# Performance work log

Hardware: AMD Instinct MI355X
Metric: run time of the kernel (lower is better)

Reference implementation:

```python
import jax, jax.numpy as jnp
import numpy as np

NUM_LABELS = 8  # static label-set size (mask values in [0, NUM_LABELS))


def setup_inputs() -> dict:
    key = jax.random.key(0)
    k1, k2, k3, k4 = jax.random.split(key, 4)
    B, C, H, W = 2, 256, 256, 256
    return {
        "c_feat": jax.random.normal(k1, (B, C, H, W), dtype=jnp.float32),
        "s_feat": jax.random.normal(k2, (B, C, H, W), dtype=jnp.float32),
        "c_mask": jax.random.randint(k3, (H, W), 0, NUM_LABELS, dtype=jnp.int64),
        "s_mask": jax.random.randint(k4, (H, W), 0, NUM_LABELS, dtype=jnp.int64),
    }


def reference(c_feat, s_feat, c_mask, s_mask):
    B, C, H, W = c_feat.shape
    cf = c_feat.reshape(B, C, H * W)            # [B, C, Nc]
    sf = s_feat.reshape(B, C, -1)               # [B, C, Ns]
    cm = c_mask.reshape(-1)                     # [Nc]
    sm = s_mask.reshape(-1)                     # [Ns]
    out = cf
    for label in range(NUM_LABELS):
        cw = (cm == label).astype(cf.dtype)     # 0/1 weights over content pixels
        sw = (sm == label).astype(sf.dtype)
        a = cw.sum()
        b = sw.sum()
        # guide-label heuristic from compute_label_info
        guide = (a > 10) & (b > 10) & (a < 10 * b) & (b < 10 * a)
        # masked content mean / centered features (zeros outside the label group)
        c_mean = (cf * cw).sum(-1) / a          # [B, C]
        c_res = (cf - c_mean[:, :, None]) * cw  # [B, C, Nc]
        cov_c = jnp.einsum('bcn,bdn->bce'.replace('e', 'd'), c_res, c_res) / (a - 1.0)
        Lc = jnp.linalg.inv(jnp.linalg.cholesky(cov_c))   # whitening (inverse Cholesky)
        # masked style statistics
        s_mean = (sf * sw).sum(-1) / b          # [B, C]
        s_res = (sf - s_mean[:, :, None]) * sw  # [B, C, Ns]
        cov_s = jnp.einsum('bcn,bdn->bcd', s_res, s_res) / (b - 1.0)
        Ls = jnp.linalg.cholesky(cov_s)                   # coloring Cholesky
        T = jnp.einsum('bcd,bde->bce', Ls, Lc)            # [B, C, C]
        colored = jnp.einsum('bce,ben->bcn', T, cf - c_mean[:, :, None]) + s_mean[:, :, None]
        sel = guide & (cm == label)             # scatter only guided label pixels
        out = jnp.where(sel[None, None, :], colored, out)
    return out.reshape(B, C, H, W)
```

## Files before the change

kernel.cpp:

```cpp
#include <hip/hip_runtime.h>
#include <stdint.h>

#define BB 2
#define CC 256
#define NN 65536
#define LL 8

#define M_CNTC 0
#define M_CNTS 8
#define M_OFFC 16
#define M_OFFS 24
#define M_CURC 32
#define M_CURS 40
#define M_GUIDE 48

typedef const __attribute__((address_space(1))) unsigned int* gp1_t;
typedef __attribute__((address_space(3))) unsigned int* lp3_t;

__device__ __forceinline__ void gload16(const float* g, float* l) {
    __builtin_amdgcn_global_load_lds((gp1_t)(const void*)g, (lp3_t)(void*)l, 16, 0, 0);
}

__global__ void k_hist(const int* __restrict__ cm, const int* __restrict__ sm,
                       int* __restrict__ meta)
{
    __shared__ int lc[LL], ls[LL];
    int t = threadIdx.x;
    if (t < LL) { lc[t] = 0; ls[t] = 0; }
    __syncthreads();
    int n = blockIdx.x * 256 + t;
    atomicAdd(&lc[cm[n] & 7], 1);
    atomicAdd(&ls[sm[n] & 7], 1);
    __syncthreads();
    if (t < LL) {
        atomicAdd(&meta[M_CNTC + t], lc[t]);
        atomicAdd(&meta[M_CNTS + t], ls[t]);
    }
}

__global__ void k_scan(int* __restrict__ meta)
{
    if (threadIdx.x == 0 && blockIdx.x == 0) {
        int oc = 0, os = 0;
        for (int l = 0; l < LL; l++) {
            meta[M_OFFC + l] = oc; meta[M_CURC + l] = oc;
            meta[M_OFFS + l] = os; meta[M_CURS + l] = os;
            oc += meta[M_CNTC + l];
            os += meta[M_CNTS + l];
        }
        for (int l = 0; l < LL; l++) {
            int a = meta[M_CNTC + l], b = meta[M_CNTS + l];
            meta[M_GUIDE + l] = (a > 10 && b > 10 && a < 10 * b && b < 10 * a) ? 1 : 0;
        }
    }
}

__global__ void k_dest(const int* __restrict__ cm, const int* __restrict__ sm,
                       int* __restrict__ meta, int* __restrict__ pdc, int* __restrict__ pds)
{
    int n = blockIdx.x * 256 + threadIdx.x;
    int lane = threadIdx.x & 63;
    unsigned long long below = (1ull << lane) - 1ull;
    int lc = cm[n] & 7, ls = sm[n] & 7;
    int dc = 0, dsv = 0;
    for (int lab = 0; lab < LL; lab++) {
        unsigned long long m = __ballot(lc == lab);
        if (m) {
            int leader = __ffsll((unsigned long long)m) - 1;
            int cntw = __popcll(m);
            int base = 0;
            if (lane == leader) base = atomicAdd(&meta[M_CURC + lab], cntw);
            base = __shfl(base, leader, 64);
            if (lc == lab) dc = base + __popcll(m & below);
        }
        unsigned long long m2 = __ballot(ls == lab);
        if (m2) {
            int leader = __ffsll((unsigned long long)m2) - 1;
            int cntw = __popcll(m2);
            int base = 0;
            if (lane == leader) base = atomicAdd(&meta[M_CURS + lab], cntw);
            base = __shfl(base, leader, 64);
            if (ls == lab) dsv = base + __popcll(m2 & below);
        }
    }
    pdc[n] = dc | (lc << 16);
    pds[n] = dsv | (ls << 16);
}

__global__ void k_gather(const float* __restrict__ feat, const int* __restrict__ pd,
                         float* __restrict__ X, float* __restrict__ sums)
{
    __shared__ float sacc[LL][256];
    int t = threadIdx.x;
    int c = blockIdx.y, b = blockIdx.z;
    int n0 = blockIdx.x * 8192;
    for (int r = 0; r < LL; r++) sacc[r][t] = 0.f;
    const float* row = feat + ((size_t)b * CC + c) * NN;
    float* Xrow = X + ((size_t)b * CC + c) * NN;
    for (int it = 0; it < 8; it++) {
        int n = n0 + it * 1024 + t * 4;
        float4 v = *(const float4*)(row + n);
        int4 pp = *(const int4*)(pd + n);
        int d0 = pp.x & 0xFFFF, l0 = pp.x >> 16;
        int d1 = pp.y & 0xFFFF, l1 = pp.y >> 16;
        int d2 = pp.z & 0xFFFF, l2 = pp.z >> 16;
        int d3 = pp.w & 0xFFFF, l3 = pp.w >> 16;
        Xrow[d0] = v.x; sacc[l0][t] += v.x;
        Xrow[d1] = v.y; sacc[l1][t] += v.y;
        Xrow[d2] = v.z; sacc[l2][t] += v.z;
        Xrow[d3] = v.w; sacc[l3][t] += v.w;
    }
    __syncthreads();
    int r = t >> 5, q = t & 31;
    float s = 0.f;
    for (int k = q; k < 256; k += 32) s += sacc[r][k];
    for (int off = 16; off; off >>= 1) s += __shfl_down(s, off, 32);
    if (q == 0) atomicAdd(&sums[((size_t)b * LL + r) * CC + c], s);
}

__global__ __launch_bounds__(256, 4) void k_syrk(const float* __restrict__ Xc, const float* __restrict__ Xs,
                                                 float* __restrict__ Raw, const int* __restrict__ meta)
{
    int z = blockIdx.z;
    int l = z & 7, b = (z >> 3) & 1, st = z >> 4;
    if (!meta[M_GUIDE + l]) return;
    int cnt = meta[(st ? M_CNTS : M_CNTC) + l];
    int off = meta[(st ? M_OFFS : M_OFFC) + l];
    int KCH = gridDim.x;
    int clen = (((cnt + KCH - 1) / KCH) + 31) & ~31;
    int p0 = off + blockIdx.x * clen;
    int lend = off + cnt;
    if (p0 >= lend) return;
    int pend = min(p0 + clen, lend);
    int y = blockIdx.y;
    int tR = (y >= 1) ? 128 : 0;
    int tC = (y == 2) ? 128 : 0;

    const float* Xb = (st ? Xs : Xc) + (size_t)b * CC * NN;

    __shared__ float As[32][132];
    __shared__ float Bs[32][132];

    int t = threadIdx.x;
    int ty = t >> 4, tx = t & 15;
    int sr = t & 31, sx = t >> 5;

    float acc[8][8];
#pragma unroll
    for (int i = 0; i < 8; i++)
#pragma unroll
        for (int j = 0; j < 8; j++) acc[i][j] = 0.f;

    for (int k0 = p0; k0 < pend; k0 += 32) {
        __syncthreads();
        int p = k0 + sx * 4;
#pragma unroll
        for (int pass = 0; pass < 4; pass++) {
            int row = pass * 32 + sr;
            const float* ap = Xb + (size_t)(tR + row) * NN + p;
            const float* bp = Xb + (size_t)(tC + row) * NN + p;
            float4 av = {0.f, 0.f, 0.f, 0.f}, bv = {0.f, 0.f, 0.f, 0.f};
            if (p + 3 < pend) { av = *(const float4*)ap; bv = *(const float4*)bp; }
            else if (p < pend) {
                int nleft = pend - p;
                for (int j = 0; j < nleft; j++) { ((float*)&av)[j] = ap[j]; ((float*)&bv)[j] = bp[j]; }
            }
            As[sx * 4 + 0][row] = av.x; As[sx * 4 + 1][row] = av.y;
            As[sx * 4 + 2][row] = av.z; As[sx * 4 + 3][row] = av.w;
            Bs[sx * 4 + 0][row] = bv.x; Bs[sx * 4 + 1][row] = bv.y;
            Bs[sx * 4 + 2][row] = bv.z; Bs[sx * 4 + 3][row] = bv.w;
        }
        __syncthreads();
#pragma unroll 4
        for (int kk = 0; kk < 32; kk++) {
            float a[8], bb[8];
#pragma unroll
            for (int i = 0; i < 8; i++) a[i] = As[kk][ty + 16 * i];
#pragma unroll
            for (int j = 0; j < 8; j++) bb[j] = Bs[kk][tx + 16 * j];
#pragma unroll
            for (int i = 0; i < 8; i++)
#pragma unroll
                for (int j = 0; j < 8; j++)
                    acc[i][j] += a[i] * bb[j];
        }
    }

    float* Mb = Raw + (size_t)z * CC * CC;
#pragma unroll
    for (int i = 0; i < 8; i++) {
        int row = tR + ty + 16 * i;
#pragma unroll
        for (int j = 0; j < 8; j++) {
            int col = tC + tx + 16 * j;
            atomicAdd(&Mb[(size_t)row * CC + col], acc[i][j]);
        }
    }
}

__global__ void k_finalize(float* __restrict__ M2c, float* __restrict__ M2s,
                           const float* __restrict__ sums_c, const float* __restrict__ sums_s,
                           const int* __restrict__ meta)
{
    int y = blockIdx.y; int l = y & 7, b = (y >> 3) & 1, st = y >> 4;
    if (!meta[M_GUIDE + l]) return;
    float a = (float)meta[(st ? M_CNTS : M_CNTC) + l];
    float* M = (st ? M2s : M2c) + ((size_t)(b * LL + l)) * CC * CC;
    const float* su = (st ? sums_s : sums_c) + ((size_t)(b * LL + l)) * CC;
    int idx = blockIdx.x * 256 + threadIdx.x;
    int row = idx >> 8, col = idx & 255;
    if (col > row) return;
    float mu_r = su[row] / a, mu_c = su[col] / a;
    M[idx] = (M[idx] - a * mu_r * mu_c) / (a - 1.f);
}

__global__ __launch_bounds__(256, 1) void k_chol(float* __restrict__ M2c, float* __restrict__ M2s,
                                                 float* __restrict__ LcT, const int* __restrict__ meta)
{
    int z = blockIdx.x; int l = z & 7, b = (z >> 3) & 1, st = z >> 4;
    if (!meta[M_GUIDE + l]) return;
    float* A = (st ? M2s : M2c) + ((size_t)(b * LL + l)) * CC * CC;
    float* Lt = st ? (float*)0 : (LcT + ((size_t)(b * LL + l)) * CC * CC);
    __shared__ float P[256][67];
    int t = threadIdx.x;
    int tyy = t >> 4, txx = t & 15;

    for (int ps = 0; ps < 4; ps++) {
        int pc = ps * 64, m = 256 - pc;
        for (int idx = t; idx < m * 64; idx += 256) {
            int r = idx >> 6, c = idx & 63;
            P[r][c] = A[(size_t)(pc + r) * CC + pc + c];
        }
        __syncthreads();
        for (int j = 0; j < 64; j++) {
            float pjj = P[j][j];
            float inv = 1.0f / sqrtf(fmaxf(pjj, 1e-20f));
            for (int r = j + 1 + t; r < m; r += 256) P[r][j] *= inv;
            __syncthreads();
            for (int r = j + 1 + t; r < m; r += 256) {
                float prj = P[r][j];
                for (int k = j + 1; k < 64; k++)
                    P[r][k] -= prj * P[k][j];
            }
            __syncthreads();
        }
        for (int idx = t; idx < m * 64; idx += 256) {
            int r = idx >> 6, c = idx & 63;
            if (c <= r) {
                float val = P[r][c];
                if (c == r) val = sqrtf(fmaxf(val, 1e-20f));
                A[(size_t)(pc + r) * CC + pc + c] = val;
                if (Lt) Lt[(size_t)(pc + c) * CC + pc + r] = val;
            }
        }
        for (int bi = ps + 1; bi < 4; bi++) {
            for (int bk = ps + 1; bk <= bi; bk++) {
                int riB = bi * 64 - pc, rkB = bk * 64 - pc;
                float accT[4][4];
#pragma unroll
                for (int u = 0; u < 4; u++)
#pragma unroll
                    for (int v = 0; v < 4; v++) accT[u][v] = 0.f;
                for (int kx = 0; kx < 64; kx++) {
                    float av[4], bv[4];
#pragma unroll
                    for (int u = 0; u < 4; u++) av[u] = P[riB + tyy * 4 + u][kx];
#pragma unroll
                    for (int v = 0; v < 4; v++) bv[v] = P[rkB + txx * 4 + v][kx];
#pragma unroll
                    for (int u = 0; u < 4; u++)
#pragma unroll
                        for (int v = 0; v < 4; v++) accT[u][v] += av[u] * bv[v];
                }
#pragma unroll
                for (int u = 0; u < 4; u++) {
                    size_t gi = bi * 64 + tyy * 4 + u;
#pragma unroll
                    for (int v = 0; v < 4; v++) {
                        size_t gk = bk * 64 + txx * 4 + v;
                        A[gi * CC + gk] -= accT[u][v];
                    }
                }
            }
        }
        __syncthreads();
    }
}

__global__ __launch_bounds__(256) void k_solve(const float* __restrict__ LcT, const float* __restrict__ M2s,
                                               float* __restrict__ TT, float* __restrict__ vv,
                                               const float* __restrict__ sums_c, const float* __restrict__ sums_s,
                                               const int* __restrict__ meta)
{
    int y = blockIdx.y; int l = y & 7;
    if (!meta[M_GUIDE + l]) return;
    const float* Lc_t = LcT + (size_t)y * CC * CC;
    const float* Ls = M2s + (size_t)y * CC * CC;
    float* Tt = TT + (size_t)y * CC * CC;
    __shared__ float m[32][257];
    __shared__ float lrow[256];
    int t = threadIdx.x;
    int g = t >> 3, tt = t & 7;
    int c = blockIdx.x * 32 + g;
    for (int i = CC - 1; i >= 0; i--) {
        lrow[t] = Lc_t[(size_t)i * CC + t];
        __syncthreads();
        if (c >= i) {
            float s = 0.f;
            for (int k = i + 1 + tt; k <= c; k += 8) s += lrow[k] * m[g][k];
            s += __shfl_down(s, 4, 8);
            s += __shfl_down(s, 2, 8);
            s += __shfl_down(s, 1, 8);
            if (tt == 0) {
                float val = (Ls[(size_t)c * CC + i] - s) / lrow[i];
                m[g][i] = val;
                Tt[(size_t)i * CC + c] = val;
            }
        }
        __syncthreads();
    }
    float aF = (float)meta[M_CNTC + l], bF = (float)meta[M_CNTS + l];
    const float* sc = sums_c + (size_t)y * CC;
    const float* ss = sums_s + (size_t)y * CC;
    float s = 0.f;
    for (int e = tt; e <= c; e += 8) s += m[g][e] * sc[e];
    s += __shfl_down(s, 4, 8);
    s += __shfl_down(s, 2, 8);
    s += __shfl_down(s, 1, 8);
    if (tt == 0) vv[(size_t)y * CC + c] = ss[c] / bF - s / aF;
}

__global__ __launch_bounds__(256, 4) void k_color(const float* __restrict__ X, const float* __restrict__ TT,
                                                  const float* __restrict__ vv, float* __restrict__ O,
                                                  const int* __restrict__ meta)
{
    int z = blockIdx.z; int b = z >> 3, l = z & 7;
    if (!meta[M_GUIDE + l]) return;
    int cnt = meta[M_CNTC + l], off = meta[M_OFFC + l];
    int lend = off + cnt;
    int p0 = off + blockIdx.x * 128;
    if (p0 >= lend) return;
    int pend = min(p0 + 128, lend);
    int c0 = blockIdx.y * 128;
    int eEnd = c0 + 128;

    __shared__ float As[32][128];
    __shared__ float Bs[32][128];

    const float* Xb = X + (size_t)b * CC * NN;
    const float* Tb = TT + ((size_t)(b * LL + l)) * CC * CC;
    const float* vb = vv + ((size_t)(b * LL + l)) * CC;
    int t = threadIdx.x;
    int ty = t >> 4, tx = t & 15;
    int w = t >> 6, ln = t & 63;
    int sr = t & 31, sx = t >> 5;
    bool safe = (p0 + 128 <= NN);

    float acc[8][8];
#pragma unroll
    for (int i = 0; i < 8; i++) {
        float vi = vb[c0 + ty + 16 * i];
#pragma unroll
        for (int j = 0; j < 8; j++) acc[i][j] = vi;
    }

    for (int e0 = 0; e0 < eEnd; e0 += 32) {
        __syncthreads();
        if (safe) {
#pragma unroll
            for (int q = 0; q < 4; q++) {
                int kk = w * 8 + q * 2 + (ln >> 5);
                int cl4 = (ln & 31) * 4;
                gload16(Tb + (size_t)(e0 + kk) * CC + c0 + cl4, &As[w * 8 + q * 2][0]);
                gload16(Xb + (size_t)(e0 + kk) * NN + p0 + cl4, &Bs[w * 8 + q * 2][0]);
            }
        } else {
#pragma unroll
            for (int pass = 0; pass < 4; pass++) {
                int cidx = pass * 32 + sx * 4;
#pragma unroll
                for (int j = 0; j < 4; j++) {
                    As[sr][cidx + j] = Tb[(size_t)(e0 + sr) * CC + c0 + cidx + j];
                    int p = p0 + cidx + j;
                    Bs[sr][cidx + j] = (p < NN) ? Xb[(size_t)(e0 + sr) * NN + p] : 0.f;
                }
            }
        }
        __syncthreads();
#pragma unroll 4
        for (int kk = 0; kk < 32; kk++) {
            float a[8], bb[8];
#pragma unroll
            for (int i = 0; i < 8; i++) a[i] = As[kk][ty + 16 * i];
#pragma unroll
            for (int j = 0; j < 8; j++) bb[j] = Bs[kk][tx + 16 * j];
#pragma unroll
            for (int i = 0; i < 8; i++)
#pragma unroll
                for (int j = 0; j < 8; j++)
                    acc[i][j] += a[i] * bb[j];
        }
    }

    float* Ob = O + (size_t)b * CC * NN;
#pragma unroll
    for (int i = 0; i < 8; i++) {
        int row = c0 + ty + 16 * i;
        float* orow = Ob + (size_t)row * NN;
#pragma unroll
        for (int j = 0; j < 8; j++) {
            int p = p0 + tx + 16 * j;
            if (p < pend) orow[p] = acc[i][j];
        }
    }
}

__global__ void k_scatter(const float* __restrict__ cf, const float* __restrict__ O,
                          const int* __restrict__ pd, float* __restrict__ out,
                          const int* __restrict__ meta)
{
    __shared__ int gd[LL];
    int t = threadIdx.x;
    if (t < LL) gd[t] = meta[M_GUIDE + t];
    __syncthreads();
    int c = blockIdx.y, b = blockIdx.z;
    int n = blockIdx.x * 1024 + t * 4;
    const float* cfr = cf + ((size_t)b * CC + c) * NN;
    const float* Or = O + ((size_t)b * CC + c) * NN;
    float4 v = *(const float4*)(cfr + n);
    int4 pp = *(const int4*)(pd + n);
    float r0 = (gd[pp.x >> 16]) ? Or[pp.x & 0xFFFF] : v.x;
    float r1 = (gd[pp.y >> 16]) ? Or[pp.y & 0xFFFF] : v.y;
    float r2 = (gd[pp.z >> 16]) ? Or[pp.z & 0xFFFF] : v.z;
    float r3 = (gd[pp.w >> 16]) ? Or[pp.w & 0xFFFF] : v.w;
    float4 r = {r0, r1, r2, r3};
    *(float4*)(out + ((size_t)b * CC + c) * NN + n) = r;
}

extern "C" void kernel_launch(void* const* d_in, const int* in_sizes, int n_in,
                              void* d_out, int out_size, void* d_ws, size_t ws_size,
                              hipStream_t stream)
{
    const float* c_feat = (const float*)d_in[0];
    const float* s_feat = (const float*)d_in[1];
    const int* cm = (const int*)d_in[2];
    const int* sm = (const int*)d_in[3];
    float* out = (float*)d_out;

    float* X2 = (float*)d_ws;
    float* M2c = X2 + (size_t)BB * CC * NN;
    float* M2s = M2c + (size_t)BB * LL * CC * CC;
    float* LcT = M2s + (size_t)BB * LL * CC * CC;
    float* T_T = LcT + (size_t)BB * LL * CC * CC;
    float* sums_c = T_T + (size_t)BB * LL * CC * CC;
    float* sums_s = sums_c + BB * LL * CC;
    float* vv = sums_s + BB * LL * CC;
    int* pdc = (int*)(vv + BB * LL * CC);
    int* pds = pdc + NN;
    int* meta = pds + NN;
    size_t need = (size_t)((char*)(meta + 64) - (char*)d_ws);
    if (ws_size < need) return;

    float* Xc = out;

    hipMemsetAsync(meta, 0, 64 * sizeof(int), stream);
    hipMemsetAsync(sums_c, 0, (size_t)2 * BB * LL * CC * sizeof(float), stream);
    hipMemsetAsync(M2c, 0, (size_t)2 * BB * LL * CC * CC * sizeof(float), stream);
    hipMemsetAsync(T_T, 0, (size_t)BB * LL * CC * CC * sizeof(float), stream);

    k_hist<<<256, 256, 0, stream>>>(cm, sm, meta);
    k_scan<<<1, 64, 0, stream>>>(meta);
    k_dest<<<256, 256, 0, stream>>>(cm, sm, meta, pdc, pds);
    k_gather<<<dim3(8, CC, BB), 256, 0, stream>>>(c_feat, pdc, Xc, sums_c);
    k_gather<<<dim3(8, CC, BB), 256, 0, stream>>>(s_feat, pds, X2, sums_s);
    k_syrk<<<dim3(16, 3, 32), 256, 0, stream>>>(Xc, X2, M2c, meta);
    k_finalize<<<dim3(256, 32), 256, 0, stream>>>(M2c, M2s, sums_c, sums_s, meta);
    k_chol<<<32, 256, 0, stream>>>(M2c, M2s, LcT, meta);
    k_solve<<<dim3(8, 16), 256, 0, stream>>>(LcT, M2s, T_T, vv, sums_c, sums_s, meta);
    k_color<<<dim3(80, 2, 16), 256, 0, stream>>>(Xc, T_T, vv, X2, meta);
    k_scatter<<<dim3(64, CC, BB), 256, 0, stream>>>(c_feat, X2, pdc, out, meta);
}
```

Measured before the change: 2.320 ms.

## Restructure Cholesky panel factorization and blocked triangular solve for T

```diff
diff --git a/kernel.cpp b/kernel.cpp
--- a/kernel.cpp
+++ b/kernel.cpp
@@ -221,52 +221,76 @@
     if (!meta[M_GUIDE + l]) return;
     float* A = (st ? M2s : M2c) + ((size_t)(b * LL + l)) * CC * CC;
     float* Lt = st ? (float*)0 : (LcT + ((size_t)(b * LL + l)) * CC * CC);
-    __shared__ float P[256][67];
+    __shared__ float P[256][33];
+    __shared__ float dinv[32];
     int t = threadIdx.x;
     int tyy = t >> 4, txx = t & 15;
 
-    for (int ps = 0; ps < 4; ps++) {
-        int pc = ps * 64, m = 256 - pc;
-        for (int idx = t; idx < m * 64; idx += 256) {
-            int r = idx >> 6, c = idx & 63;
+    for (int ps = 0; ps < 8; ps++) {
+        int pc = ps * 32, m = 256 - pc;
+        for (int idx = t; idx < m * 32; idx += 256) {
+            int r = idx >> 5, c = idx & 31;
             P[r][c] = A[(size_t)(pc + r) * CC + pc + c];
         }
         __syncthreads();
-        for (int j = 0; j < 64; j++) {
-            float pjj = P[j][j];
-            float inv = 1.0f / sqrtf(fmaxf(pjj, 1e-20f));
-            for (int r = j + 1 + t; r < m; r += 256) P[r][j] *= inv;
-            __syncthreads();
-            for (int r = j + 1 + t; r < m; r += 256) {
-                float prj = P[r][j];
-                for (int k = j + 1; k < 64; k++)
-                    P[r][k] -= prj * P[k][j];
-            }
-            __syncthreads();
-        }
-        for (int idx = t; idx < m * 64; idx += 256) {
-            int r = idx >> 6, c = idx & 63;
-            if (c <= r) {
+
+        if (t < 64) {
+            volatile float* Pv = &P[0][0];
+            int lane = t;
+            for (int j = 0; j < 32; j++) {
+                float pjj = Pv[j * 33 + j];
+                float ljj = sqrtf(fmaxf(pjj, 1e-20f));
+                float inv = 1.0f / ljj;
+                if (lane == j) { Pv[j * 33 + j] = ljj; dinv[j] = inv; }
+                if (lane > j && lane < 32) {
+                    float sc = Pv[lane * 33 + j] * inv;
+                    Pv[lane * 33 + j] = sc;
+                    for (int k = j + 1; k <= lane; k++)
+                        Pv[lane * 33 + k] -= sc * Pv[k * 33 + j];
+                }
+            }
+        }
+        __syncthreads();
+
+        for (int r = 32 + t; r < m; r += 256) {
+            for (int j = 0; j < 32; j++) {
+                float s = P[r][j];
+                for (int k = 0; k < j; k++) s -= P[r][k] * P[j][k];
+                P[r][j] = s * dinv[j];
+            }
+        }
+        __syncthreads();
+
+        for (int idx = t; idx < m * 32; idx += 256) {
+            int r = idx >> 5, c = idx & 31;
+            if (r >= 32 || c <= r) {
                 float val = P[r][c];
-                if (c == r) val = sqrtf(fmaxf(val, 1e-20f));
                 A[(size_t)(pc + r) * CC + pc + c] = val;
                 if (Lt) Lt[(size_t)(pc + c) * CC + pc + r] = val;
             }
         }
-        for (int bi = ps + 1; bi < 4; bi++) {
-            for (int bk = ps + 1; bk <= bi; bk++) {
-                int riB = bi * 64 - pc, rkB = bk * 64 - pc;
+
+        int m2 = m - 32;
+        int nb = (m2 + 63) >> 6;
+        for (int bi2 = 0; bi2 < nb; bi2++) {
+            for (int bk2 = 0; bk2 <= bi2; bk2++) {
+                int ri[4], ci[4];
+#pragma unroll
+                for (int u = 0; u < 4; u++) {
+                    ri[u] = min(32 + bi2 * 64 + tyy * 4 + u, m - 1);
+                    ci[u] = min(32 + bk2 * 64 + txx * 4 + u, m - 1);
+                }
                 float accT[4][4];
 #pragma unroll
                 for (int u = 0; u < 4; u++)
 #pragma unroll
                     for (int v = 0; v < 4; v++) accT[u][v] = 0.f;
-                for (int kx = 0; kx < 64; kx++) {
+                for (int kx = 0; kx < 32; kx++) {
                     float av[4], bv[4];
 #pragma unroll
-                    for (int u = 0; u < 4; u++) av[u] = P[riB + tyy * 4 + u][kx];
-#pragma unroll
-                    for (int v = 0; v < 4; v++) bv[v] = P[rkB + txx * 4 + v][kx];
+                    for (int u = 0; u < 4; u++) av[u] = P[ri[u]][kx];
+#pragma unroll
+                    for (int v = 0; v < 4; v++) bv[v] = P[ci[v]][kx];
 #pragma unroll
                     for (int u = 0; u < 4; u++)
 #pragma unroll
@@ -274,11 +298,14 @@
                 }
 #pragma unroll
                 for (int u = 0; u < 4; u++) {
-                    size_t gi = bi * 64 + tyy * 4 + u;
-#pragma unroll
-                    for (int v = 0; v < 4; v++) {
-                        size_t gk = bk * 64 + txx * 4 + v;
-                        A[gi * CC + gk] -= accT[u][v];
+                    int gi = 32 + bi2 * 64 + tyy * 4 + u;
+                    if (gi < m) {
+#pragma unroll
+                        for (int v = 0; v < 4; v++) {
+                            int gk = 32 + bk2 * 64 + txx * 4 + v;
+                            if (gk < m && gk <= gi)
+                                A[(size_t)(pc + gi) * CC + pc + gk] -= accT[u][v];
+                        }
                     }
                 }
             }
@@ -287,47 +314,82 @@
     }
 }
 
-__global__ __launch_bounds__(256) void k_solve(const float* __restrict__ LcT, const float* __restrict__ M2s,
-                                               float* __restrict__ TT, float* __restrict__ vv,
-                                               const float* __restrict__ sums_c, const float* __restrict__ sums_s,
-                                               const int* __restrict__ meta)
-{
-    int y = blockIdx.y; int l = y & 7;
+__global__ __launch_bounds__(256, 1) void k_solve(const float* __restrict__ LcT, const float* __restrict__ M2s,
+                                                  float* TT, float* __restrict__ vv,
+                                                  const float* __restrict__ sums_c, const float* __restrict__ sums_s,
+                                                  const int* __restrict__ meta)
+{
+    int y = blockIdx.x; int l = y & 7;
     if (!meta[M_GUIDE + l]) return;
-    const float* Lc_t = LcT + (size_t)y * CC * CC;
+    const float* U = LcT + (size_t)y * CC * CC;
     const float* Ls = M2s + (size_t)y * CC * CC;
     float* Tt = TT + (size_t)y * CC * CC;
-    __shared__ float m[32][257];
-    __shared__ float lrow[256];
-    int t = threadIdx.x;
-    int g = t >> 3, tt = t & 7;
-    int c = blockIdx.x * 32 + g;
-    for (int i = CC - 1; i >= 0; i--) {
-        lrow[t] = Lc_t[(size_t)i * CC + t];
-        __syncthreads();
-        if (c >= i) {
-            float s = 0.f;
-            for (int k = i + 1 + tt; k <= c; k += 8) s += lrow[k] * m[g][k];
-            s += __shfl_down(s, 4, 8);
-            s += __shfl_down(s, 2, 8);
-            s += __shfl_down(s, 1, 8);
-            if (tt == 0) {
-                float val = (Ls[(size_t)c * CC + i] - s) / lrow[i];
-                m[g][i] = val;
-                Tt[(size_t)i * CC + c] = val;
-            }
+    __shared__ float xs[64][257];
+    __shared__ float Ut[64][68];
+    __shared__ float dinv[64];
+    __shared__ float scl[256];
+    int t = threadIdx.x, c = t;
+    scl[t] = sums_c[(size_t)y * CC + t];
+    float vacc = 0.f;
+
+    for (int bi = 3; bi >= 0; bi--) {
+        int gi0 = bi * 64;
+        for (int idx = t; idx < 64 * 256; idx += 256) {
+            int cc = idx >> 6, i = idx & 63;
+            float vL = Ls[(size_t)cc * CC + gi0 + i];
+            xs[i][cc] = (gi0 + i > cc) ? 0.f : vL;
+        }
+        __syncthreads();
+        for (int bj = bi + 1; bj < 4; bj++) {
+            for (int idx = t; idx < 64 * 64; idx += 256) {
+                int r = idx >> 6, k = idx & 63;
+                Ut[r][k] = U[(size_t)(gi0 + r) * CC + bj * 64 + k];
+            }
+            __syncthreads();
+            float xk[64];
+#pragma unroll
+            for (int k = 0; k < 64; k++) xk[k] = Tt[(size_t)(bj * 64 + k) * CC + c];
+            for (int r = 0; r < 64; r++) {
+                float sum = 0.f;
+#pragma unroll
+                for (int k = 0; k < 64; k++) sum += Ut[r][k] * xk[k];
+                xs[r][c] -= sum;
+            }
+            __syncthreads();
+        }
+        for (int idx = t; idx < 64 * 64; idx += 256) {
+            int r = idx >> 6, k = idx & 63;
+            float uv = (k >= r) ? U[(size_t)(gi0 + r) * CC + gi0 + k] : 0.f;
+            Ut[r][k] = uv;
+            if (k == r) dinv[r] = 1.0f / uv;
+        }
+        __syncthreads();
+        for (int s = 7; s >= 0; s--) {
+            int r0 = s * 8;
+            for (int r = r0 + 7; r >= r0; r--) {
+                float sum = xs[r][c];
+                for (int k = r + 1; k < r0 + 8; k++) sum -= Ut[r][k] * xs[k][c];
+                xs[r][c] = sum * dinv[r];
+            }
+            float xq[8];
+#pragma unroll
+            for (int q = 0; q < 8; q++) xq[q] = xs[r0 + q][c];
+            for (int r = 0; r < r0; r++) {
+                float sum = Ut[r][r0] * xq[0];
+#pragma unroll
+                for (int q = 1; q < 8; q++) sum += Ut[r][r0 + q] * xq[q];
+                xs[r][c] -= sum;
+            }
+        }
+        for (int r = 0; r < 64; r++) {
+            float xv = xs[r][c];
+            Tt[(size_t)(gi0 + r) * CC + c] = xv;
+            vacc += xv * scl[gi0 + r];
         }
         __syncthreads();
     }
     float aF = (float)meta[M_CNTC + l], bF = (float)meta[M_CNTS + l];
-    const float* sc = sums_c + (size_t)y * CC;
-    const float* ss = sums_s + (size_t)y * CC;
-    float s = 0.f;
-    for (int e = tt; e <= c; e += 8) s += m[g][e] * sc[e];
-    s += __shfl_down(s, 4, 8);
-    s += __shfl_down(s, 2, 8);
-    s += __shfl_down(s, 1, 8);
-    if (tt == 0) vv[(size_t)y * CC + c] = ss[c] / bF - s / aF;
+    vv[(size_t)y * CC + c] = sums_s[(size_t)y * CC + c] / bF - vacc / aF;
 }
 
 __global__ __launch_bounds__(256, 4) void k_color(const float* __restrict__ X, const float* __restrict__ TT,
@@ -466,7 +528,6 @@
     hipMemsetAsync(meta, 0, 64 * sizeof(int), stream);
     hipMemsetAsync(sums_c, 0, (size_t)2 * BB * LL * CC * sizeof(float), stream);
     hipMemsetAsync(M2c, 0, (size_t)2 * BB * LL * CC * CC * sizeof(float), stream);
-    hipMemsetAsync(T_T, 0, (size_t)BB * LL * CC * CC * sizeof(float), stream);
 
     k_hist<<<256, 256, 0, stream>>>(cm, sm, meta);
     k_scan<<<1, 64, 0, stream>>>(meta);
@@ -476,7 +537,7 @@
     k_syrk<<<dim3(16, 3, 32), 256, 0, stream>>>(Xc, X2, M2c, meta);
     k_finalize<<<dim3(256, 32), 256, 0, stream>>>(M2c, M2s, sums_c, sums_s, meta);
     k_chol<<<32, 256, 0, stream>>>(M2c, M2s, LcT, meta);
-    k_solve<<<dim3(8, 16), 256, 0, stream>>>(LcT, M2s, T_T, vv, sums_c, sums_s, meta);
+    k_solve<<<16, 256, 0, stream>>>(LcT, M2s, T_T, vv, sums_c, sums_s, meta);
     k_color<<<dim3(80, 2, 16), 256, 0, stream>>>(Xc, T_T, vv, X2, meta);
     k_scatter<<<dim3(64, CC, BB), 256, 0, stream>>>(c_feat, X2, pdc, out, meta);
 }
```

Result: slower. 2.614 ms (+12.6%).
